# Kernel tuning notes

Measured on AMD Instinct MI355X. Metric: run time of the kernel, lower is better.

## Reference

```python
import jax, jax.numpy as jnp
import numpy as np

C_T = 64
C_OUT = 128
RANK = 8
LN_EPS = 1e-5


def setup_inputs() -> dict:
    key = jax.random.key(0)
    ks = jax.random.split(key, 8)
    B, L = 1, 768
    feat = jax.random.normal(ks[0], (B, L, L, C_T), dtype=jnp.float32)
    Wq = jax.random.normal(ks[1], (C_T, 1), dtype=jnp.float32) / np.sqrt(C_T)
    bq = jnp.zeros((1,), dtype=jnp.float32)
    ln_g = jnp.ones((C_T * 3,), dtype=jnp.float32)
    ln_b = jnp.zeros((C_T * 3,), dtype=jnp.float32)
    WU = jax.random.normal(ks[2], (C_T * 3, RANK * C_OUT), dtype=jnp.float32) / np.sqrt(C_T * 3)
    bU = jnp.zeros((RANK * C_OUT,), dtype=jnp.float32)
    WV = jax.random.normal(ks[3], (C_T * 3, RANK * C_OUT), dtype=jnp.float32) / np.sqrt(C_T * 3)
    bV = jnp.zeros((RANK * C_OUT,), dtype=jnp.float32)
    sigma = jnp.ones((RANK,), dtype=jnp.float32)
    return {"template_feat": feat, "Wq": Wq, "bq": bq, "ln_g": ln_g, "ln_b": ln_b,
            "WU": WU, "bU": bU, "WV": WV, "bV": bV, "sigma": sigma}


def _layer_norm(x, g, b):
    mu = jnp.mean(x, axis=-1, keepdims=True)
    var = jnp.mean(jnp.square(x - mu), axis=-1, keepdims=True)
    return (x - mu) * jax.lax.rsqrt(var + LN_EPS) * g + b


def reference(template_feat, Wq, bq, ln_g, ln_b, WU, bU, WV, bV, sigma):
    B, L, _, C = template_feat.shape
    rank = sigma.shape[0]
    c_out = WU.shape[1] // rank
    # attention logits, shared by both pools: [B, L, L]
    logits = jnp.einsum('bijc,co->bijo', template_feat, Wq)[..., 0] + bq[0]
    # row pool: softmax over j (dim=2)
    w_row = jax.nn.softmax(logits, axis=2)
    row_feat = jnp.einsum('bij,bijc->bic', w_row, template_feat)
    # col pool: softmax over i (dim=1)
    w_col = jax.nn.softmax(logits, axis=1)
    col_feat = jnp.einsum('bij,bijc->bjc', w_col, template_feat)
    # diagonal gather: [B, L, C]
    idx = jnp.arange(L)
    diag_feat = template_feat[:, idx, idx, :]
    left = _layer_norm(jnp.concatenate([diag_feat, row_feat, col_feat], axis=-1), ln_g, ln_b)
    right = _layer_norm(jnp.concatenate([diag_feat, col_feat, row_feat], axis=-1), ln_g, ln_b)
    template_left = (left @ WU + bU).reshape(B, L, rank, c_out)
    template_right = (right @ WV + bV).reshape(B, L, rank, c_out)
    template_left = template_left * sigma[None, None, :, None]
    return (template_left, template_right)
```

## Files before the change

### kernel.cpp

```cpp
#include <hip/hip_runtime.h>
#include <math.h>

#define LL 768
#define CT 64
#define KD 192
#define OC 1024
#define TS 16
#define NST 48
#define PCH 68

__device__ __forceinline__ float sum16(float x) {
    x += __int_as_float(__builtin_amdgcn_update_dpp(0, __float_as_int(x), 0xB1, 0xF, 0xF, true));
    x += __int_as_float(__builtin_amdgcn_update_dpp(0, __float_as_int(x), 0x4E, 0xF, 0xF, true));
    x += __int_as_float(__builtin_amdgcn_update_dpp(0, __float_as_int(x), 0x124, 0xF, 0xF, true));
    x += __int_as_float(__builtin_amdgcn_update_dpp(0, __float_as_int(x), 0x128, 0xF, 0xF, true));
    return x;
}

__global__ __launch_bounds__(256, 6) void k_fused(const float* __restrict__ feat,
                                                  const float* __restrict__ Wq,
                                                  const float* __restrict__ bq,
                                                  float* __restrict__ rp,
                                                  float* __restrict__ cp) {
    __shared__ float4 lbuf[16][8][17];
    __shared__ float  zb[16][9];

    int t = threadIdx.x;
    int u = t >> 4, q = t & 15;
    int bi = blockIdx.x, bj = blockIdx.y;
    int i0 = bi * TS, j0 = bj * TS;

    const float4 wq = *reinterpret_cast<const float4*>(Wq + q * 4);
    const float bqv = bq[0];

    const float* fb = feat + ((size_t)i0 * LL + j0 + u) * CT + q * 4;
    const size_t istr = (size_t)LL * CT;
    float4 creg = make_float4(0.f, 0.f, 0.f, 0.f);
    float zc = 0.f;

    float4 fnext = *reinterpret_cast<const float4*>(fb);

    #pragma unroll 2
    for (int half = 0; half < 2; ++half) {
        #pragma unroll
        for (int ii = 0; ii < 8; ++ii) {
            const int idx = half * 8 + ii;
            const float4 f = fnext;
            if (idx < 15)
                fnext = *reinterpret_cast<const float4*>(fb + (size_t)(idx + 1) * istr);

            float s = f.x * wq.x + f.y * wq.y + f.z * wq.z + f.w * wq.w;
            s = sum16(s);
            float e = __expf(s + bqv);

            float4 p;
            p.x = e * f.x; p.y = e * f.y; p.z = e * f.z; p.w = e * f.w;

            creg.x += p.x; creg.y += p.y; creg.z += p.z; creg.w += p.w;
            zc += e;

            lbuf[u][ii][q] = p;
            if (q == 0) zb[u][ii] = e;
        }
        __syncthreads();

        if (t < 128) {
            int ii = t >> 4, c4 = t & 15;
            float4 a = make_float4(0.f, 0.f, 0.f, 0.f);
            #pragma unroll
            for (int uu = 0; uu < 16; ++uu) {
                const float4 v = lbuf[uu][ii][c4];
                a.x += v.x; a.y += v.y; a.z += v.z; a.w += v.w;
            }
            *reinterpret_cast<float4*>(rp + ((size_t)bj * LL + i0 + half * 8 + ii) * PCH
                                       + c4 * 4) = a;
        }
        if (t < 8) {
            float zz = 0.f;
            #pragma unroll
            for (int uu = 0; uu < 16; ++uu) zz += zb[uu][t];
            rp[((size_t)bj * LL + i0 + half * 8 + t) * PCH + 64] = zz;
        }
        __syncthreads();
    }

    size_t cpo = ((size_t)bi * LL + (j0 + u)) * PCH;
    *reinterpret_cast<float4*>(cp + cpo + q * 4) = creg;
    if (q == 0) cp[cpo + 64] = zc;
}

__global__ __launch_bounds__(256) void k_combine(const float* __restrict__ rp,
                                                 const float* __restrict__ cp,
                                                 float* __restrict__ rcfeat) {
    int t = threadIdx.x;
    int r = t >> 4, q = t & 15;
    int L0 = blockIdx.x * 16;
    int side = blockIdx.y;
    const float* base = side ? cp : rp;

    float4 acc = make_float4(0.f, 0.f, 0.f, 0.f);
    float z = 0.f;
    #pragma unroll 4
    for (int s = 0; s < NST; ++s) {
        const float* p = base + ((size_t)s * LL + L0 + r) * PCH;
        const float4 v = *reinterpret_cast<const float4*>(p + q * 4);
        acc.x += v.x; acc.y += v.y; acc.z += v.z; acc.w += v.w;
        z += p[64];
    }
    float inv = 1.0f / z;
    acc.x *= inv; acc.y *= inv; acc.z *= inv; acc.w *= inv;
    *reinterpret_cast<float4*>(rcfeat + (size_t)side * LL * CT
                               + (L0 + r) * CT + q * 4) = acc;
}

__global__ __launch_bounds__(256) void k_final(const float* __restrict__ feat,
                                               const float* __restrict__ rcfeat,
                                               const float* __restrict__ ln_g,
                                               const float* __restrict__ ln_b,
                                               const float* __restrict__ WU,
                                               const float* __restrict__ bU,
                                               const float* __restrict__ WV,
                                               const float* __restrict__ bV,
                                               const float* __restrict__ sigma,
                                               float* __restrict__ out) {
    __shared__ float xbuf[8][KD];
    int t = threadIdx.x;
    int wid = t >> 6, l = t & 63;
    int r0 = blockIdx.x * 8;
    int right = blockIdx.y;
    const float* rfeat = rcfeat;
    const float* cfeat = rcfeat + LL * CT;

    for (int r = wid; r < 8; r += 4) {
        int i = r0 + r;
        float d  = feat[((size_t)i * LL + i) * CT + l];
        float rv = rfeat[(size_t)i * CT + l];
        float cv = cfeat[(size_t)i * CT + l];
        float sum = d + rv + cv;
        #pragma unroll
        for (int o = 32; o; o >>= 1) sum += __shfl_xor(sum, o);
        float mu = sum * (1.0f / 192.0f);
        float d0 = d - mu, d1 = rv - mu, d2 = cv - mu;
        float sq = d0 * d0 + d1 * d1 + d2 * d2;
        #pragma unroll
        for (int o = 32; o; o >>= 1) sq += __shfl_xor(sq, o);
        float rstd = rsqrtf(sq * (1.0f / 192.0f) + 1e-5f);
        float h0 = d0 * rstd, h1 = d1 * rstd, h2 = d2 * rstd;
        float a1 = right ? h2 : h1;
        float a2 = right ? h1 : h2;
        xbuf[r][l]       = h0 * ln_g[l]       + ln_b[l];
        xbuf[r][64 + l]  = a1 * ln_g[64 + l]  + ln_b[64 + l];
        xbuf[r][128 + l] = a2 * ln_g[128 + l] + ln_b[128 + l];
    }
    __syncthreads();

    const float* W    = right ? WV : WU;
    const float* bias = right ? bV : bU;
    int o = t * 4;
    float4 acc[8];
    #pragma unroll
    for (int r = 0; r < 8; ++r) acc[r] = make_float4(0.f, 0.f, 0.f, 0.f);

    for (int k = 0; k < KD; k += 4) {
        float4 xr[8];
        #pragma unroll
        for (int r = 0; r < 8; ++r)
            xr[r] = *reinterpret_cast<const float4*>(&xbuf[r][k]);
        #pragma unroll
        for (int kk = 0; kk < 4; ++kk) {
            float4 wv = *reinterpret_cast<const float4*>(W + (size_t)(k + kk) * OC + o);
            #pragma unroll
            for (int r = 0; r < 8; ++r) {
                float xv = (&xr[r].x)[kk];
                acc[r].x = fmaf(xv, wv.x, acc[r].x);
                acc[r].y = fmaf(xv, wv.y, acc[r].y);
                acc[r].z = fmaf(xv, wv.z, acc[r].z);
                acc[r].w = fmaf(xv, wv.w, acc[r].w);
            }
        }
    }

    float4 bb = *reinterpret_cast<const float4*>(bias + o);
    float sg = right ? 1.0f : sigma[o >> 7];
    float* obase = out + (right ? (size_t)LL * OC : 0);
    #pragma unroll
    for (int r = 0; r < 8; ++r) {
        float4 v;
        v.x = (acc[r].x + bb.x) * sg;
        v.y = (acc[r].y + bb.y) * sg;
        v.z = (acc[r].z + bb.z) * sg;
        v.w = (acc[r].w + bb.w) * sg;
        *reinterpret_cast<float4*>(obase + (size_t)(r0 + r) * OC + o) = v;
    }
}

extern "C" void kernel_launch(void* const* d_in, const int* in_sizes, int n_in,
                              void* d_out, int out_size, void* d_ws, size_t ws_size,
                              hipStream_t stream) {
    const float* feat  = (const float*)d_in[0];
    const float* Wq    = (const float*)d_in[1];
    const float* bq    = (const float*)d_in[2];
    const float* ln_g  = (const float*)d_in[3];
    const float* ln_b  = (const float*)d_in[4];
    const float* WU    = (const float*)d_in[5];
    const float* bU    = (const float*)d_in[6];
    const float* WV    = (const float*)d_in[7];
    const float* bV    = (const float*)d_in[8];
    const float* sigma = (const float*)d_in[9];
    float* out = (float*)d_out;

    float* ws     = (float*)d_ws;
    float* rp     = ws;
    float* cp     = rp + (size_t)NST * LL * PCH;
    float* rcfeat = cp + (size_t)NST * LL * PCH;

    hipLaunchKernelGGL(k_fused, dim3(NST, NST), dim3(256), 0, stream,
                       feat, Wq, bq, rp, cp);
    hipLaunchKernelGGL(k_combine, dim3(NST, 2), dim3(256), 0, stream,
                       rp, cp, rcfeat);
    hipLaunchKernelGGL(k_final, dim3(LL / 8, 2), dim3(256), 0, stream,
                       feat, rcfeat, ln_g, ln_b, WU, bU, WV, bV, sigma, out);
}
```

Measured before the change: 75.59 us.

## Fuse partial-sum combine into final kernel and deepen feature prefetch

Removes the separate combine kernel: each final-projection block now reduces the row/column partial sums for its 8 rows into shared memory before the layer norm, saving a launch and the rcfeat round-trip. Both the left and right blocks redo this reduction, so the partial-sum reads double. The fused pooling kernel now keeps four feature loads in flight through rotating registers instead of one. Its occupancy hint drops from 6 to 4 blocks to give it more registers.

```diff
diff --git a/kernel.cpp b/kernel.cpp
--- a/kernel.cpp
+++ b/kernel.cpp
@@ -17,7 +17,7 @@
     return x;
 }
 
-__global__ __launch_bounds__(256, 6) void k_fused(const float* __restrict__ feat,
+__global__ __launch_bounds__(256, 4) void k_fused(const float* __restrict__ feat,
                                                   const float* __restrict__ Wq,
                                                   const float* __restrict__ bq,
                                                   float* __restrict__ rp,
@@ -38,16 +38,21 @@
     float4 creg = make_float4(0.f, 0.f, 0.f, 0.f);
     float zc = 0.f;
 
-    float4 fnext = *reinterpret_cast<const float4*>(fb);
-
-    #pragma unroll 2
+    float4 fr0 = *reinterpret_cast<const float4*>(fb + 0 * istr);
+    float4 fr1 = *reinterpret_cast<const float4*>(fb + 1 * istr);
+    float4 fr2 = *reinterpret_cast<const float4*>(fb + 2 * istr);
+    float4 fr3 = *reinterpret_cast<const float4*>(fb + 3 * istr);
+
+    #pragma unroll
     for (int half = 0; half < 2; ++half) {
         #pragma unroll
         for (int ii = 0; ii < 8; ++ii) {
             const int idx = half * 8 + ii;
-            const float4 f = fnext;
-            if (idx < 15)
-                fnext = *reinterpret_cast<const float4*>(fb + (size_t)(idx + 1) * istr);
+            float4 f;
+            if ((idx & 3) == 0) { f = fr0; if (idx + 4 < 16) fr0 = *reinterpret_cast<const float4*>(fb + (size_t)(idx + 4) * istr); }
+            else if ((idx & 3) == 1) { f = fr1; if (idx + 4 < 16) fr1 = *reinterpret_cast<const float4*>(fb + (size_t)(idx + 4) * istr); }
+            else if ((idx & 3) == 2) { f = fr2; if (idx + 4 < 16) fr2 = *reinterpret_cast<const float4*>(fb + (size_t)(idx + 4) * istr); }
+            else                     { f = fr3; if (idx + 4 < 16) fr3 = *reinterpret_cast<const float4*>(fb + (size_t)(idx + 4) * istr); }
 
             float s = f.x * wq.x + f.y * wq.y + f.z * wq.z + f.w * wq.w;
             s = sum16(s);
@@ -89,32 +94,9 @@
     if (q == 0) cp[cpo + 64] = zc;
 }
 
-__global__ __launch_bounds__(256) void k_combine(const float* __restrict__ rp,
-                                                 const float* __restrict__ cp,
-                                                 float* __restrict__ rcfeat) {
-    int t = threadIdx.x;
-    int r = t >> 4, q = t & 15;
-    int L0 = blockIdx.x * 16;
-    int side = blockIdx.y;
-    const float* base = side ? cp : rp;
-
-    float4 acc = make_float4(0.f, 0.f, 0.f, 0.f);
-    float z = 0.f;
-    #pragma unroll 4
-    for (int s = 0; s < NST; ++s) {
-        const float* p = base + ((size_t)s * LL + L0 + r) * PCH;
-        const float4 v = *reinterpret_cast<const float4*>(p + q * 4);
-        acc.x += v.x; acc.y += v.y; acc.z += v.z; acc.w += v.w;
-        z += p[64];
-    }
-    float inv = 1.0f / z;
-    acc.x *= inv; acc.y *= inv; acc.z *= inv; acc.w *= inv;
-    *reinterpret_cast<float4*>(rcfeat + (size_t)side * LL * CT
-                               + (L0 + r) * CT + q * 4) = acc;
-}
-
 __global__ __launch_bounds__(256) void k_final(const float* __restrict__ feat,
-                                               const float* __restrict__ rcfeat,
+                                               const float* __restrict__ rp,
+                                               const float* __restrict__ cp,
                                                const float* __restrict__ ln_g,
                                                const float* __restrict__ ln_b,
                                                const float* __restrict__ WU,
@@ -123,19 +105,39 @@
                                                const float* __restrict__ bV,
                                                const float* __restrict__ sigma,
                                                float* __restrict__ out) {
+    __shared__ float cf2[2][8][68];
     __shared__ float xbuf[8][KD];
     int t = threadIdx.x;
-    int wid = t >> 6, l = t & 63;
     int r0 = blockIdx.x * 8;
     int right = blockIdx.y;
-    const float* rfeat = rcfeat;
-    const float* cfeat = rcfeat + LL * CT;
-
+
+    {
+        int side = t >> 7;
+        int r = (t >> 4) & 7, q = t & 15;
+        const float* base = side ? cp : rp;
+        float4 acc = make_float4(0.f, 0.f, 0.f, 0.f);
+        float z = 0.f;
+        #pragma unroll 4
+        for (int s = 0; s < NST; ++s) {
+            const float* p = base + ((size_t)s * LL + r0 + r) * PCH;
+            const float4 v = *reinterpret_cast<const float4*>(p + q * 4);
+            acc.x += v.x; acc.y += v.y; acc.z += v.z; acc.w += v.w;
+            z += p[64];
+        }
+        float inv = 1.0f / z;
+        cf2[side][r][q * 4 + 0] = acc.x * inv;
+        cf2[side][r][q * 4 + 1] = acc.y * inv;
+        cf2[side][r][q * 4 + 2] = acc.z * inv;
+        cf2[side][r][q * 4 + 3] = acc.w * inv;
+    }
+    __syncthreads();
+
+    int wid = t >> 6, l = t & 63;
     for (int r = wid; r < 8; r += 4) {
         int i = r0 + r;
         float d  = feat[((size_t)i * LL + i) * CT + l];
-        float rv = rfeat[(size_t)i * CT + l];
-        float cv = cfeat[(size_t)i * CT + l];
+        float rv = cf2[0][r][l];
+        float cv = cf2[1][r][l];
         float sum = d + rv + cv;
         #pragma unroll
         for (int o = 32; o; o >>= 1) sum += __shfl_xor(sum, o);
@@ -209,15 +211,12 @@
     const float* sigma = (const float*)d_in[9];
     float* out = (float*)d_out;
 
-    float* ws     = (float*)d_ws;
-    float* rp     = ws;
-    float* cp     = rp + (size_t)NST * LL * PCH;
-    float* rcfeat = cp + (size_t)NST * LL * PCH;
+    float* ws = (float*)d_ws;
+    float* rp = ws;
+    float* cp = rp + (size_t)NST * LL * PCH;
 
     hipLaunchKernelGGL(k_fused, dim3(NST, NST), dim3(256), 0, stream,
                        feat, Wq, bq, rp, cp);
-    hipLaunchKernelGGL(k_combine, dim3(NST, 2), dim3(256), 0, stream,
-                       rp, cp, rcfeat);
     hipLaunchKernelGGL(k_final, dim3(LL / 8, 2), dim3(256), 0, stream,
-                       feat, rcfeat, ln_g, ln_b, WU, bU, WV, bV, sigma, out);
-}
+                       feat, rp, cp, ln_g, ln_b, WU, bU, WV, bV, sigma, out);
+}
```

Result: slower. 84.76 us (+12.1%).
